# Optimization experiments

Measured on AMD Instinct MI355X. Metric: run time of the kernel, lower is better.

## Reference

```python
import jax, jax.numpy as jnp
import numpy as np

EPS = 1e-5

def _layernorm(x, w, b):
    # LayerNorm over (C,F,S) per batch element, affine params shape [C,F,S]
    m = jnp.mean(x, axis=(1, 2, 3), keepdims=True)
    v = jnp.mean((x - m) ** 2, axis=(1, 2, 3), keepdims=True)
    return (x - m) * jax.lax.rsqrt(v + EPS) * w + b

def _pconv(x, w, b):
    # 1x1 conv == channel GEMM: w [O,C], x [B,C,F,S]
    return jnp.einsum('oc,bcfs->bofs', w, x) + b[:, None, None]

def setup_inputs() -> dict:
    C, F, S, B = 64, 256, 256, 4
    key = jax.random.key(0)
    ks = jax.random.split(key, 16)
    sc = 0.05
    return {
        'x': jax.random.normal(ks[0], (B, C, F, S), jnp.float32),
        'ln1_w': jnp.ones((C, F, S), jnp.float32),
        'ln1_b': jnp.zeros((C, F, S), jnp.float32),
        'ln2_w': jnp.ones((C, F, S), jnp.float32),
        'ln2_b': jnp.zeros((C, F, S), jnp.float32),
        'w1': jax.random.normal(ks[1], (2 * C, C), jnp.float32) * sc,
        'b1': jnp.zeros((2 * C,), jnp.float32),
        'dw_w': jax.random.normal(ks[2], (2 * C,), jnp.float32) * sc + 1.0,
        'dw_b': jnp.zeros((2 * C,), jnp.float32),
        'attn_w1': jax.random.normal(ks[3], (C, C), jnp.float32) * sc,
        'attn_b1': jnp.zeros((C,), jnp.float32),
        'attn_w2': jax.random.normal(ks[4], (C, C), jnp.float32) * sc,
        'attn_b2': jnp.zeros((C,), jnp.float32),
        'w2': jax.random.normal(ks[5], (C, C), jnp.float32) * sc,
        'b2': jnp.zeros((C,), jnp.float32),
        'w3': jax.random.normal(ks[6], (2 * C, C), jnp.float32) * sc,
        'b3': jnp.zeros((2 * C,), jnp.float32),
        'w4': jax.random.normal(ks[7], (C, C), jnp.float32) * sc,
        'b4': jnp.zeros((C,), jnp.float32),
    }

def reference(x, ln1_w, ln1_b, ln2_w, ln2_b, w1, b1, dw_w, dw_b,
              attn_w1, attn_b1, attn_w2, attn_b2, w2, b2, w3, b3, w4, b4):
    # branch 1: norm -> 1x1 conv (C->2C) -> depthwise 1x1 -> GLU -> channel attn -> 1x1 conv
    h = _layernorm(x, ln1_w, ln1_b)
    h = _pconv(h, w1, b1)
    h = h * dw_w[:, None, None] + dw_b[:, None, None]  # 1x1 depthwise = per-channel affine
    a, g = jnp.split(h, 2, axis=1)
    h = a * jax.nn.sigmoid(g)  # GLU over channel dim
    # channel attention (SE-style, reduction_ratio=1)
    p = jnp.mean(h, axis=(2, 3))  # [B,C]
    s = jax.nn.sigmoid(jax.nn.relu(p @ attn_w1.T + attn_b1) @ attn_w2.T + attn_b2)
    h = h * s[:, :, None, None]
    h = _pconv(h, w2, b2)
    y = h + x
    # branch 2: norm -> 1x1 conv (C->2C) -> GLU -> 1x1 conv
    h2 = _layernorm(y, ln2_w, ln2_b)
    h2 = _pconv(h2, w3, b3)
    a2, g2 = jnp.split(h2, 2, axis=1)
    h2 = a2 * jax.nn.sigmoid(g2)
    h2 = _pconv(h2, w4, b4)
    return h2 + y
```

## Files before the change

kernel.cpp:

```cpp
#include <hip/hip_runtime.h>
#include <cstdint>
#include <cstddef>

#define CH 64
#define NP 65536
#define NPB 1024
constexpr float EPS_LN = 1e-5f;

using f32x4  = __attribute__((ext_vector_type(4))) float;
using bf16x8 = __attribute__((ext_vector_type(8))) short;
using s16x4  = __attribute__((ext_vector_type(4))) short;
using s16x2  = __attribute__((ext_vector_type(2))) short;

__device__ __forceinline__ short f2bf(float f){
  union { float f; uint32_t u; } v; v.f = f;
  uint32_t r = v.u + 0x7FFFu + ((v.u >> 16) & 1u);
  return (short)(r >> 16);
}
__device__ __forceinline__ float bf2f(short s){
  union { uint32_t u; float f; } v; v.u = ((uint32_t)(uint16_t)s) << 16;
  return v.f;
}
__device__ __forceinline__ float sigmoidf_(float x){ return 1.f/(1.f+__expf(-x)); }

__device__ __forceinline__ void lds_barrier(){
  asm volatile("s_waitcnt lgkmcnt(0)\n\ts_barrier" ::: "memory");
}

__global__ __launch_bounds__(256) void k_prep(
    const float* __restrict__ x,
    const float* __restrict__ w1, const float* __restrict__ w2,
    const float* __restrict__ w3, const float* __restrict__ w4,
    float* __restrict__ xstat, short* __restrict__ wbf)
{
  int blk = blockIdx.x, tid = threadIdx.x;
  if (blk < 1024) {
    int b = blk >> 8, chunk = blk & 255;
    const float* base = x + (size_t)b*CH*NP + (size_t)chunk*16384;
    float s = 0.f, s2 = 0.f;
    for (int i = tid*4; i < 16384; i += 1024) {
      f32x4 v = *(const f32x4*)(base + i);
      s  += v.x + v.y + v.z + v.w;
      s2 += v.x*v.x + v.y*v.y + v.z*v.z + v.w*v.w;
    }
    for (int d=1; d<64; d<<=1){ s += __shfl_xor(s,d,64); s2 += __shfl_xor(s2,d,64); }
    __shared__ float ls[8];
    int wv = tid>>6;
    if ((tid&63)==0){ ls[wv]=s; ls[4+wv]=s2; }
    __syncthreads();
    if (tid==0){
      xstat[blk*2]   = ls[0]+ls[1]+ls[2]+ls[3];
      xstat[blk*2+1] = ls[4]+ls[5]+ls[6]+ls[7];
    }
  } else {
    int wblk = blk - 1024;
    const float* src; short* dst; int off;
    if (wblk < 8)       { src = w1; dst = wbf;         off = wblk*1024; }
    else if (wblk < 12) { src = w2; dst = wbf + 8192;  off = (wblk-8)*1024; }
    else if (wblk < 20) { src = w3; dst = wbf + 12288; off = (wblk-12)*1024; }
    else                { src = w4; dst = wbf + 20480; off = (wblk-20)*1024; }
    for (int i = tid; i < 1024; i += 256) dst[off+i] = f2bf(src[off+i]);
  }
}

__global__ void k_fin1(const float* __restrict__ xstat, float* __restrict__ stats1){
  int b = threadIdx.x >> 6, lane = threadIdx.x & 63;
  float s=0.f, s2=0.f;
  #pragma unroll
  for (int j=0;j<4;j++){
    int i = b*256 + j*64 + lane;
    s += xstat[i*2]; s2 += xstat[i*2+1];
  }
  for (int d=1; d<64; d<<=1){ s += __shfl_xor(s,d,64); s2 += __shfl_xor(s2,d,64); }
  if (lane==0){
    float m = s*(1.f/4194304.f);
    float v = s2*(1.f/4194304.f) - m*m;
    stats1[b]=m; stats1[4+b]=rsqrtf(v+EPS_LN);
  }
}

__global__ __launch_bounds__(256,4) void k_branch1(
    const float* __restrict__ x, const float* __restrict__ lnw, const float* __restrict__ lnb,
    const short* __restrict__ w1bf, const float* __restrict__ b1,
    const float* __restrict__ dww, const float* __restrict__ dwb,
    const float* __restrict__ stats1, short* __restrict__ hglu, float* __restrict__ ppart)
{
  int blk = blockIdx.x;
  int b = blk >> 8;
  int tile0 = (blk & 255) * 4;
  int tid = threadIdx.x, wv = tid>>6, lane = tid&63, l = lane&15, q = lane>>4;
  int c_ = tid>>4, p4 = tid&15;
  float mean = stats1[b], rstd = stats1[4+b];
  const float* xb = x + (size_t)b*CH*NP;
  short* hb = hglu + (size_t)b*CH*NP;

  __shared__ __align__(16) short wlds[8192];
  __shared__ __align__(16) short lin[64*78];
  __shared__ float pacc[4][64];
  __shared__ __align__(16) float cc[128];

  #pragma unroll
  for (int g0=0; g0<4; g0++){
    int g = g0*256 + tid;
    int mt = g>>7, ks = (g>>6)&1, qq = (g>>4)&3, ll = g&15;
    int m = mt*16 + ll;
    float sc = dww[m];
    bf16x8 w8 = *(const bf16x8*)(w1bf + (m*CH + ks*32 + qq*8));
    #pragma unroll
    for (int j=0;j<8;j++) w8[j] = f2bf(bf2f(w8[j]) * sc);
    *(bf16x8*)(&wlds[g*8]) = w8;
  }
  if (tid < 128) cc[tid] = b1[tid]*dww[tid] + dwb[tid];

  f32x4 pX[4], pW[4], pB[4];
  #pragma unroll
  for (int it=0; it<4; it++){
    int c = it*16 + c_;
    size_t o = (size_t)c*NP + tile0*64 + p4*4;
    pX[it] = *(const f32x4*)(xb + o);
    pW[it] = *(const f32x4*)(lnw + o);
    pB[it] = *(const f32x4*)(lnb + o);
  }

  float rsum[16];
  #pragma unroll
  for (int i=0;i<16;i++) rsum[i] = 0.f;

  for (int t=0; t<4; t++){
    int pos0 = (tile0 + t)*64;
    #pragma unroll
    for (int it=0; it<4; it++){
      int c = it*16 + c_;
      s16x2 lo, hi;
      lo[0] = f2bf((pX[it][0]-mean)*rstd*pW[it][0] + pB[it][0]);
      lo[1] = f2bf((pX[it][1]-mean)*rstd*pW[it][1] + pB[it][1]);
      hi[0] = f2bf((pX[it][2]-mean)*rstd*pW[it][2] + pB[it][2]);
      hi[1] = f2bf((pX[it][3]-mean)*rstd*pW[it][3] + pB[it][3]);
      *(s16x2*)(&lin[c*78 + p4*4])     = lo;
      *(s16x2*)(&lin[c*78 + p4*4 + 2]) = hi;
    }
    if (t < 3){
      #pragma unroll
      for (int it=0; it<4; it++){
        int c = it*16 + c_;
        size_t o = (size_t)c*NP + pos0 + 64 + p4*4;
        pX[it] = *(const f32x4*)(xb + o);
        pW[it] = *(const f32x4*)(lnw + o);
        pB[it] = *(const f32x4*)(lnb + o);
      }
    }
    lds_barrier();

    bf16x8 bfrag[2];
    #pragma unroll
    for (int ks=0; ks<2; ks++)
      #pragma unroll
      for (int j=0; j<8; j++)
        bfrag[ks][j] = lin[(ks*32+q*8+j)*78 + wv*16 + l];

    f32x4 acc[8];
    #pragma unroll
    for (int mt=0; mt<8; mt++){
      f32x4 a = {0.f,0.f,0.f,0.f};
      #pragma unroll
      for (int ks=0; ks<2; ks++){
        bf16x8 af = *(const bf16x8*)(&wlds[(mt*128 + ks*64 + q*16 + l)*8]);
        a = __builtin_amdgcn_mfma_f32_16x16x32_bf16(af, bfrag[ks], a, 0, 0, 0);
      }
      acc[mt] = a;
    }

    int pos = pos0 + wv*16 + l;
    #pragma unroll
    for (int mt=0; mt<4; mt++){
      f32x4 ccA = *(const f32x4*)(&cc[mt*16 + q*4]);
      f32x4 ccG = *(const f32x4*)(&cc[64 + mt*16 + q*4]);
      s16x4 pk;
      #pragma unroll
      for (int r=0; r<4; r++){
        float av = acc[mt][r]   + ccA[r];
        float gv = acc[mt+4][r] + ccG[r];
        float h = av * sigmoidf_(gv);
        rsum[mt*4+r] += h;
        pk[r] = f2bf(h);
      }
      *(s16x4*)(hb + (size_t)pos*CH + mt*16 + q*4) = pk;
    }
    lds_barrier();
  }

  #pragma unroll
  for (int i=0;i<16;i++){
    float v = rsum[i];
    v += __shfl_xor(v,1,64); v += __shfl_xor(v,2,64);
    v += __shfl_xor(v,4,64); v += __shfl_xor(v,8,64);
    if (l==0) pacc[wv][(i>>2)*16 + q*4 + (i&3)] = v;
  }
  lds_barrier();
  if (tid < 64){
    float s = pacc[0][tid]+pacc[1][tid]+pacc[2][tid]+pacc[3][tid];
    ppart[((size_t)b*256 + (blk & 255))*64 + tid] = s;
  }
}

__global__ __launch_bounds__(1024) void k_attn(
    const float* __restrict__ ppart,
    const float* __restrict__ aw1, const float* __restrict__ ab1,
    const float* __restrict__ aw2, const float* __restrict__ ab2,
    const short* __restrict__ w2bf, short* __restrict__ w2s)
{
  int b = blockIdx.x, t = threadIdx.x;
  int c = t & 63, seg = t >> 6;
  __shared__ float awl1[64*65], awl2[64*65];
  __shared__ float pl[16][64];
  __shared__ float parr[64], t1a[64], sarr[64];

  #pragma unroll
  for (int k=0;k<4;k++){
    int i = t + k*1024;
    int row = i >> 6, col = i & 63;
    awl1[row*65 + col] = aw1[i];
    awl2[row*65 + col] = aw2[i];
  }
  const float* pb = ppart + (size_t)b*256*64;
  float s = 0.f;
  #pragma unroll
  for (int k=0;k<16;k++) s += pb[(seg*16 + k)*64 + c];
  pl[seg][c] = s;
  __syncthreads();
  if (t < 64){
    float acc = 0.f;
    #pragma unroll
    for (int j=0;j<16;j++) acc += pl[j][t];
    parr[t] = acc * (1.f/65536.f);
  }
  __syncthreads();
  if (t < 64){
    float acc = ab1[t];
    #pragma unroll
    for (int k=0;k<64;k++) acc += awl1[t*65+k]*parr[k];
    t1a[t] = fmaxf(acc, 0.f);
  }
  __syncthreads();
  if (t < 64){
    float acc = ab2[t];
    #pragma unroll
    for (int k=0;k<64;k++) acc += awl2[t*65+k]*t1a[k];
    sarr[t] = sigmoidf_(acc);
  }
  __syncthreads();
  #pragma unroll
  for (int k=0;k<4;k++){
    int i = t + k*1024;
    w2s[b*4096 + i] = f2bf(bf2f(w2bf[i]) * sarr[i & 63]);
  }
}

__global__ __launch_bounds__(256,4) void k_mid(
    const short* __restrict__ hglu, const short* __restrict__ w2s,
    const float* __restrict__ b2, const float* __restrict__ x,
    float* __restrict__ y, float* __restrict__ ystat)
{
  int blk = blockIdx.x;
  int b = blk >> 8;
  int tile0 = (blk & 255) * 4;
  int tid = threadIdx.x, wv = tid>>6, lane = tid&63, l = lane&15, q = lane>>4;
  int c_ = tid>>4, p4 = tid&15;
  const short* hb = hglu + (size_t)b*CH*NP;
  const float* xb = x + (size_t)b*CH*NP;
  float* yb = y + (size_t)b*CH*NP;
  int posl = wv*16 + l;

  __shared__ __align__(16) short w2l[4096];
  __shared__ __align__(16) float lout[64*65];

  #pragma unroll
  for (int g0=0; g0<2; g0++){
    int g = g0*256 + tid;
    int mt = g>>7, ks = (g>>6)&1, qq = (g>>4)&3, ll = g&15;
    *(bf16x8*)(&w2l[g*8]) = *(const bf16x8*)(w2s + b*4096 + (mt*16+ll)*CH + ks*32 + qq*8);
  }
  float b2v[4];
  #pragma unroll
  for (int it=0; it<4; it++) b2v[it] = b2[it*16 + c_];

  bf16x8 pH0, pH1; f32x4 pXr[4];
  {
    const short* hr = hb + (size_t)(tile0*64 + posl)*CH;
    pH0 = *(const bf16x8*)(hr + q*8);
    pH1 = *(const bf16x8*)(hr + 32 + q*8);
    #pragma unroll
    for (int it=0; it<4; it++)
      pXr[it] = *(const f32x4*)(xb + (size_t)(it*16+c_)*NP + tile0*64 + p4*4);
  }
  lds_barrier();

  float s1 = 0.f, s2 = 0.f;

  for (int t=0; t<4; t++){
    int pos0 = (tile0 + t)*64;
    bf16x8 h0 = pH0, h1 = pH1;
    if (t < 3){
      const short* hr = hb + (size_t)(pos0 + 64 + posl)*CH;
      pH0 = *(const bf16x8*)(hr + q*8);
      pH1 = *(const bf16x8*)(hr + 32 + q*8);
    }
    f32x4 acc[4];
    #pragma unroll
    for (int mt=0; mt<4; mt++){
      f32x4 a = {0.f,0.f,0.f,0.f};
      a = __builtin_amdgcn_mfma_f32_16x16x32_bf16(
            *(const bf16x8*)(&w2l[(mt*128 + 0*64 + q*16 + l)*8]), h0, a, 0,0,0);
      a = __builtin_amdgcn_mfma_f32_16x16x32_bf16(
            *(const bf16x8*)(&w2l[(mt*128 + 1*64 + q*16 + l)*8]), h1, a, 0,0,0);
      acc[mt] = a;
    }
    #pragma unroll
    for (int mt=0; mt<4; mt++)
      #pragma unroll
      for (int r=0; r<4; r++)
        lout[posl*65 + mt*16 + q*4 + r] = acc[mt][r];
    lds_barrier();

    f32x4 yv[4];
    #pragma unroll
    for (int it=0; it<4; it++){
      int c = it*16 + c_;
      #pragma unroll
      for (int j=0; j<4; j++){
        float v = lout[(p4*4+j)*65 + c] + b2v[it] + pXr[it][j];
        yv[it][j] = v; s1 += v; s2 += v*v;
      }
    }
    if (t < 3){
      #pragma unroll
      for (int it=0; it<4; it++)
        pXr[it] = *(const f32x4*)(xb + (size_t)(it*16+c_)*NP + pos0 + 64 + p4*4);
    }
    #pragma unroll
    for (int it=0; it<4; it++)
      *(f32x4*)(yb + (size_t)(it*16+c_)*NP + pos0 + p4*4) = yv[it];
    lds_barrier();
  }

  for (int d=1; d<64; d<<=1){ s1 += __shfl_xor(s1,d,64); s2 += __shfl_xor(s2,d,64); }
  __shared__ float red[8];
  if (lane==0){ red[wv]=s1; red[4+wv]=s2; }
  __syncthreads();
  if (tid==0){
    ystat[(size_t)blk*2]   = red[0]+red[1]+red[2]+red[3];
    ystat[(size_t)blk*2+1] = red[4]+red[5]+red[6]+red[7];
  }
}

__global__ void k_fin2(const float* __restrict__ ystat, float* __restrict__ stats2){
  int t = threadIdx.x;
  int b = t >> 6, lane = t & 63;
  float s=0.f, s2=0.f;
  #pragma unroll
  for (int j=0;j<4;j++){
    int e = b*256 + j*64 + lane;
    s  += ystat[e*2];
    s2 += ystat[e*2+1];
  }
  for (int d=1; d<64; d<<=1){ s += __shfl_xor(s,d,64); s2 += __shfl_xor(s2,d,64); }
  if (lane==0){
    float m = s*(1.f/4194304.f);
    float v = s2*(1.f/4194304.f) - m*m;
    stats2[b]=m; stats2[4+b]=rsqrtf(v+EPS_LN);
  }
}

__global__ __launch_bounds__(256,3) void k_branch2(
    float* __restrict__ yio, const float* __restrict__ lnw, const float* __restrict__ lnb,
    const short* __restrict__ w3bf, const float* __restrict__ b3,
    const short* __restrict__ w4bf, const float* __restrict__ b4,
    const float* __restrict__ stats2)
{
  int blk = blockIdx.x;
  int b = blk >> 8;
  int tile0 = (blk & 255) * 4;
  int tid = threadIdx.x, wv = tid>>6, lane = tid&63, l = lane&15, q = lane>>4;
  int c_ = tid>>4, p4 = tid&15;
  float mean = stats2[b], rstd = stats2[4+b];
  float* yb = yio + (size_t)b*CH*NP;
  int posl = wv*16 + l;

  __shared__ __align__(16) short w3l[8192];
  __shared__ __align__(16) short w4l[4096];
  __shared__ __align__(16) short lin[64*78];
  __shared__ __align__(16) char lun[64*65*4];
  short* lglu = (short*)lun;
  float* lout = (float*)lun;
  __shared__ __align__(16) float b3l[128];

  #pragma unroll
  for (int g0=0; g0<4; g0++){
    int g = g0*256 + tid;
    int mt = g>>7, ks = (g>>6)&1, qq = (g>>4)&3, ll = g&15;
    *(bf16x8*)(&w3l[g*8]) = *(const bf16x8*)(w3bf + ((mt*16+ll)*CH + ks*32 + qq*8));
  }
  #pragma unroll
  for (int g0=0; g0<2; g0++){
    int g = g0*256 + tid;
    int mt = g>>7, ks = (g>>6)&1, qq = (g>>4)&3, ll = g&15;
    *(bf16x8*)(&w4l[g*8]) = *(const bf16x8*)(w4bf + ((mt*16+ll)*CH + ks*32 + qq*8));
  }
  if (tid < 128) b3l[tid] = b3[tid];
  float b4v[4];
  #pragma unroll
  for (int it=0; it<4; it++) b4v[it] = b4[it*16 + c_];

  f32x4 pY[4], pW[4], pB[4];
  #pragma unroll
  for (int it=0; it<4; it++){
    int c = it*16 + c_;
    size_t o = (size_t)c*NP + tile0*64 + p4*4;
    pY[it] = *(const f32x4*)(yb + o);
    pW[it] = *(const f32x4*)(lnw + o);
    pB[it] = *(const f32x4*)(lnb + o);
  }

  for (int t=0; t<4; t++){
    int pos0 = (tile0 + t)*64;
    #pragma unroll
    for (int it=0; it<4; it++){
      int c = it*16 + c_;
      s16x2 lo, hi;
      lo[0] = f2bf((pY[it][0]-mean)*rstd*pW[it][0] + pB[it][0]);
      lo[1] = f2bf((pY[it][1]-mean)*rstd*pW[it][1] + pB[it][1]);
      hi[0] = f2bf((pY[it][2]-mean)*rstd*pW[it][2] + pB[it][2]);
      hi[1] = f2bf((pY[it][3]-mean)*rstd*pW[it][3] + pB[it][3]);
      *(s16x2*)(&lin[c*78 + p4*4])     = lo;
      *(s16x2*)(&lin[c*78 + p4*4 + 2]) = hi;
    }
    if (t < 3){
      #pragma unroll
      for (int it=0; it<4; it++){
        int c = it*16 + c_;
        size_t o = (size_t)c*NP + pos0 + 64 + p4*4;
        pW[it] = *(const f32x4*)(lnw + o);
        pB[it] = *(const f32x4*)(lnb + o);
      }
    }
    lds_barrier();

    bf16x8 bfrag[2];
    #pragma unroll
    for (int ks=0; ks<2; ks++)
      #pragma unroll
      for (int j=0; j<8; j++)
        bfrag[ks][j] = lin[(ks*32+q*8+j)*78 + wv*16 + l];

    f32x4 acc[8];
    #pragma unroll
    for (int mt=0; mt<8; mt++){
      f32x4 a = {0.f,0.f,0.f,0.f};
      #pragma unroll
      for (int ks=0; ks<2; ks++){
        bf16x8 af = *(const bf16x8*)(&w3l[(mt*128 + ks*64 + q*16 + l)*8]);
        a = __builtin_amdgcn_mfma_f32_16x16x32_bf16(af, bfrag[ks], a, 0, 0, 0);
      }
      acc[mt] = a;
    }

    #pragma unroll
    for (int mt=0; mt<4; mt++){
      f32x4 bA = *(const f32x4*)(&b3l[mt*16 + q*4]);
      f32x4 bG = *(const f32x4*)(&b3l[64 + mt*16 + q*4]);
      s16x4 pk;
      #pragma unroll
      for (int r=0; r<4; r++){
        float av = acc[mt][r]   + bA[r];
        float gv = acc[mt+4][r] + bG[r];
        pk[r] = f2bf(av * sigmoidf_(gv));
      }
      *(s16x4*)(&lglu[posl*72 + mt*16 + q*4]) = pk;
    }
    lds_barrier();

    bf16x8 pfrag[2];
    pfrag[0] = *(const bf16x8*)(&lglu[posl*72 + q*8]);
    pfrag[1] = *(const bf16x8*)(&lglu[posl*72 + 32 + q*8]);
    lds_barrier();

    f32x4 acc2[4];
    #pragma unroll
    for (int mt=0; mt<4; mt++){
      f32x4 a = {0.f,0.f,0.f,0.f};
      #pragma unroll
      for (int ks=0; ks<2; ks++){
        bf16x8 af = *(const bf16x8*)(&w4l[(mt*128 + ks*64 + q*16 + l)*8]);
        a = __builtin_amdgcn_mfma_f32_16x16x32_bf16(af, ks ? pfrag[1] : pfrag[0], a, 0, 0, 0);
      }
      acc2[mt] = a;
    }
    #pragma unroll
    for (int mt=0; mt<4; mt++)
      #pragma unroll
      for (int r=0; r<4; r++)
        lout[posl*65 + mt*16 + q*4 + r] = acc2[mt][r];
    lds_barrier();

    f32x4 yv[4];
    #pragma unroll
    for (int it=0; it<4; it++){
      int c = it*16 + c_;
      #pragma unroll
      for (int j=0; j<4; j++)
        yv[it][j] = lout[(p4*4+j)*65 + c] + b4v[it] + pY[it][j];
    }
    if (t < 3){
      #pragma unroll
      for (int it=0; it<4; it++){
        int c = it*16 + c_;
        pY[it] = *(const f32x4*)(yb + (size_t)c*NP + pos0 + 64 + p4*4);
      }
    }
    #pragma unroll
    for (int it=0; it<4; it++)
      *(f32x4*)(yb + (size_t)(it*16+c_)*NP + pos0 + p4*4) = yv[it];
  }
}

extern "C" void kernel_launch(void* const* d_in, const int* in_sizes, int n_in,
                              void* d_out, int out_size, void* d_ws, size_t ws_size,
                              hipStream_t stream){
  const float* x    = (const float*)d_in[0];
  const float* ln1w = (const float*)d_in[1];
  const float* ln1b = (const float*)d_in[2];
  const float* ln2w = (const float*)d_in[3];
  const float* ln2b = (const float*)d_in[4];
  const float* w1   = (const float*)d_in[5];
  const float* b1   = (const float*)d_in[6];
  const float* dww  = (const float*)d_in[7];
  const float* dwb  = (const float*)d_in[8];
  const float* aw1  = (const float*)d_in[9];
  const float* ab1  = (const float*)d_in[10];
  const float* aw2  = (const float*)d_in[11];
  const float* ab2  = (const float*)d_in[12];
  const float* w2   = (const float*)d_in[13];
  const float* b2   = (const float*)d_in[14];
  const float* w3   = (const float*)d_in[15];
  const float* b3   = (const float*)d_in[16];
  const float* w4   = (const float*)d_in[17];
  const float* b4   = (const float*)d_in[18];
  float* out = (float*)d_out;
  float* ws  = (float*)d_ws;

  float* xstat  = ws;
  float* stats1 = ws + 2048;
  float* ystat  = ws + 2112;
  float* stats2 = ws + 10304;
  short* wbf    = (short*)(ws + 10368);
  short* w2s    = (short*)(ws + 22656);
  float* ppart  = ws + 30848;
  short* hglu   = (short*)(ws + 292992);

  hipLaunchKernelGGL(k_prep,    dim3(1048), dim3(256),  0, stream, x, w1, w2, w3, w4, xstat, wbf);
  hipLaunchKernelGGL(k_fin1,    dim3(1),    dim3(256),  0, stream, xstat, stats1);
  hipLaunchKernelGGL(k_branch1, dim3(1024), dim3(256),  0, stream, x, ln1w, ln1b, wbf, b1, dww, dwb, stats1, hglu, ppart);
  hipLaunchKernelGGL(k_attn,    dim3(4),    dim3(1024), 0, stream, ppart, aw1, ab1, aw2, ab2, wbf + 8192, w2s);
  hipLaunchKernelGGL(k_mid,     dim3(1024), dim3(256),  0, stream, hglu, w2s, b2, x, out, ystat);
  hipLaunchKernelGGL(k_fin2,    dim3(1),    dim3(256),  0, stream, ystat, stats2);
  hipLaunchKernelGGL(k_branch2, dim3(1024), dim3(256),  0, stream, out, ln2w, ln2b, wbf + 12288, b3, wbf + 20480, b4, stats2);
}
```

Baseline: 281.5 us.

## Make each wave own its position tile and drop block barriers in GEMM loops

Restructures branch1, mid and branch2 so each wavefront loads, normalizes and transposes its own 16-position slice through a private LDS region. Block-wide barriers inside the loop become per-wave lgkmcnt waits. Per-wave LDS buffers are smaller, and branch2 is split across twice as many blocks. The intent is to remove s_barrier stalls and lift occupancy and parallelism, at the cost of narrower 64-byte global access segments per channel row and LN weight loads no longer prefetched.

```diff
diff --git a/kernel.cpp b/kernel.cpp
--- a/kernel.cpp
+++ b/kernel.cpp
@@ -4,13 +4,11 @@
 
 #define CH 64
 #define NP 65536
-#define NPB 1024
 constexpr float EPS_LN = 1e-5f;
 
 using f32x4  = __attribute__((ext_vector_type(4))) float;
 using bf16x8 = __attribute__((ext_vector_type(8))) short;
 using s16x4  = __attribute__((ext_vector_type(4))) short;
-using s16x2  = __attribute__((ext_vector_type(2))) short;
 
 __device__ __forceinline__ short f2bf(float f){
   union { float f; uint32_t u; } v; v.f = f;
@@ -25,6 +23,9 @@
 
 __device__ __forceinline__ void lds_barrier(){
   asm volatile("s_waitcnt lgkmcnt(0)\n\ts_barrier" ::: "memory");
+}
+__device__ __forceinline__ void wave_fence(){
+  asm volatile("s_waitcnt lgkmcnt(0)" ::: "memory");
 }
 
 __global__ __launch_bounds__(256) void k_prep(
@@ -87,17 +88,17 @@
 {
   int blk = blockIdx.x;
   int b = blk >> 8;
-  int tile0 = (blk & 255) * 4;
   int tid = threadIdx.x, wv = tid>>6, lane = tid&63, l = lane&15, q = lane>>4;
-  int c_ = tid>>4, p4 = tid&15;
+  int base = (blk & 255)*256 + wv*64;
   float mean = stats1[b], rstd = stats1[4+b];
   const float* xb = x + (size_t)b*CH*NP;
   short* hb = hglu + (size_t)b*CH*NP;
 
   __shared__ __align__(16) short wlds[8192];
-  __shared__ __align__(16) short lin[64*78];
+  __shared__ __align__(16) float cc[128];
   __shared__ float pacc[4][64];
-  __shared__ __align__(16) float cc[128];
+  __shared__ __align__(16) short linS[4][1280];
+  short* lin = linS[wv];
 
   #pragma unroll
   for (int g0=0; g0<4; g0++){
@@ -112,51 +113,43 @@
   }
   if (tid < 128) cc[tid] = b1[tid]*dww[tid] + dwb[tid];
 
-  f32x4 pX[4], pW[4], pB[4];
-  #pragma unroll
-  for (int it=0; it<4; it++){
-    int c = it*16 + c_;
-    size_t o = (size_t)c*NP + tile0*64 + p4*4;
-    pX[it] = *(const f32x4*)(xb + o);
-    pW[it] = *(const f32x4*)(lnw + o);
-    pB[it] = *(const f32x4*)(lnb + o);
-  }
+  f32x4 pX[4];
+  #pragma unroll
+  for (int it=0; it<4; it++)
+    pX[it] = *(const f32x4*)(xb + (size_t)(it*16+l)*NP + base + q*4);
+  lds_barrier();
 
   float rsum[16];
   #pragma unroll
-  for (int i=0;i<16;i++) rsum[i] = 0.f;
-
+  for (int i=0;i<16;i++) rsum[i]=0.f;
+
+  #pragma unroll
   for (int t=0; t<4; t++){
-    int pos0 = (tile0 + t)*64;
+    int pos_w = base + t*16;
     #pragma unroll
     for (int it=0; it<4; it++){
-      int c = it*16 + c_;
-      s16x2 lo, hi;
-      lo[0] = f2bf((pX[it][0]-mean)*rstd*pW[it][0] + pB[it][0]);
-      lo[1] = f2bf((pX[it][1]-mean)*rstd*pW[it][1] + pB[it][1]);
-      hi[0] = f2bf((pX[it][2]-mean)*rstd*pW[it][2] + pB[it][2]);
-      hi[1] = f2bf((pX[it][3]-mean)*rstd*pW[it][3] + pB[it][3]);
-      *(s16x2*)(&lin[c*78 + p4*4])     = lo;
-      *(s16x2*)(&lin[c*78 + p4*4 + 2]) = hi;
+      int c = it*16 + l;
+      size_t o = (size_t)c*NP + pos_w + q*4;
+      f32x4 lw4 = *(const f32x4*)(lnw + o);
+      f32x4 lb4 = *(const f32x4*)(lnb + o);
+      s16x4 pk;
+      #pragma unroll
+      for (int j=0;j<4;j++) pk[j] = f2bf((pX[it][j]-mean)*rstd*lw4[j] + lb4[j]);
+      *(s16x4*)(&lin[c*20 + q*4]) = pk;
     }
     if (t < 3){
       #pragma unroll
-      for (int it=0; it<4; it++){
-        int c = it*16 + c_;
-        size_t o = (size_t)c*NP + pos0 + 64 + p4*4;
-        pX[it] = *(const f32x4*)(xb + o);
-        pW[it] = *(const f32x4*)(lnw + o);
-        pB[it] = *(const f32x4*)(lnb + o);
-      }
-    }
-    lds_barrier();
+      for (int it=0; it<4; it++)
+        pX[it] = *(const f32x4*)(xb + (size_t)(it*16+l)*NP + pos_w + 16 + q*4);
+    }
+    wave_fence();
 
     bf16x8 bfrag[2];
     #pragma unroll
     for (int ks=0; ks<2; ks++)
       #pragma unroll
       for (int j=0; j<8; j++)
-        bfrag[ks][j] = lin[(ks*32+q*8+j)*78 + wv*16 + l];
+        bfrag[ks][j] = lin[(ks*32 + q*8 + j)*20 + l];
 
     f32x4 acc[8];
     #pragma unroll
@@ -170,7 +163,6 @@
       acc[mt] = a;
     }
 
-    int pos = pos0 + wv*16 + l;
     #pragma unroll
     for (int mt=0; mt<4; mt++){
       f32x4 ccA = *(const f32x4*)(&cc[mt*16 + q*4]);
@@ -184,9 +176,8 @@
         rsum[mt*4+r] += h;
         pk[r] = f2bf(h);
       }
-      *(s16x4*)(hb + (size_t)pos*CH + mt*16 + q*4) = pk;
-    }
-    lds_barrier();
+      *(s16x4*)(hb + (size_t)(pos_w + l)*CH + mt*16 + q*4) = pk;
+    }
   }
 
   #pragma unroll
@@ -196,7 +187,7 @@
     v += __shfl_xor(v,4,64); v += __shfl_xor(v,8,64);
     if (l==0) pacc[wv][(i>>2)*16 + q*4 + (i&3)] = v;
   }
-  lds_barrier();
+  __syncthreads();
   if (tid < 64){
     float s = pacc[0][tid]+pacc[1][tid]+pacc[2][tid]+pacc[3][tid];
     ppart[((size_t)b*256 + (blk & 255))*64 + tid] = s;
@@ -263,16 +254,15 @@
 {
   int blk = blockIdx.x;
   int b = blk >> 8;
-  int tile0 = (blk & 255) * 4;
   int tid = threadIdx.x, wv = tid>>6, lane = tid&63, l = lane&15, q = lane>>4;
-  int c_ = tid>>4, p4 = tid&15;
+  int base = (blk & 255)*256 + wv*64;
   const short* hb = hglu + (size_t)b*CH*NP;
   const float* xb = x + (size_t)b*CH*NP;
   float* yb = y + (size_t)b*CH*NP;
-  int posl = wv*16 + l;
 
   __shared__ __align__(16) short w2l[4096];
-  __shared__ __align__(16) float lout[64*65];
+  __shared__ __align__(16) float foutS[4][1088];
+  float* fout = foutS[wv];
 
   #pragma unroll
   for (int g0=0; g0<2; g0++){
@@ -282,26 +272,26 @@
   }
   float b2v[4];
   #pragma unroll
-  for (int it=0; it<4; it++) b2v[it] = b2[it*16 + c_];
-
-  bf16x8 pH0, pH1; f32x4 pXr[4];
+  for (int it=0; it<4; it++) b2v[it] = b2[it*16 + l];
+
+  bf16x8 pH0, pH1; f32x4 pX[4];
   {
-    const short* hr = hb + (size_t)(tile0*64 + posl)*CH;
+    const short* hr = hb + (size_t)(base + l)*CH;
     pH0 = *(const bf16x8*)(hr + q*8);
     pH1 = *(const bf16x8*)(hr + 32 + q*8);
     #pragma unroll
     for (int it=0; it<4; it++)
-      pXr[it] = *(const f32x4*)(xb + (size_t)(it*16+c_)*NP + tile0*64 + p4*4);
+      pX[it] = *(const f32x4*)(xb + (size_t)(it*16+l)*NP + base + q*4);
   }
   lds_barrier();
 
-  float s1 = 0.f, s2 = 0.f;
-
+  float s1=0.f, s2=0.f;
+  #pragma unroll
   for (int t=0; t<4; t++){
-    int pos0 = (tile0 + t)*64;
+    int pos_w = base + t*16;
     bf16x8 h0 = pH0, h1 = pH1;
     if (t < 3){
-      const short* hr = hb + (size_t)(pos0 + 64 + posl)*CH;
+      const short* hr = hb + (size_t)(pos_w + 16 + l)*CH;
       pH0 = *(const bf16x8*)(hr + q*8);
       pH1 = *(const bf16x8*)(hr + 32 + q*8);
     }
@@ -317,30 +307,27 @@
     }
     #pragma unroll
     for (int mt=0; mt<4; mt++)
-      #pragma unroll
-      for (int r=0; r<4; r++)
-        lout[posl*65 + mt*16 + q*4 + r] = acc[mt][r];
-    lds_barrier();
+      *(f32x4*)(&fout[l*68 + mt*16 + q*4]) = acc[mt];
+    wave_fence();
 
     f32x4 yv[4];
     #pragma unroll
     for (int it=0; it<4; it++){
-      int c = it*16 + c_;
-      #pragma unroll
-      for (int j=0; j<4; j++){
-        float v = lout[(p4*4+j)*65 + c] + b2v[it] + pXr[it][j];
+      int c = it*16 + l;
+      #pragma unroll
+      for (int j=0;j<4;j++){
+        float v = fout[(q*4+j)*68 + c] + b2v[it] + pX[it][j];
         yv[it][j] = v; s1 += v; s2 += v*v;
       }
     }
     if (t < 3){
       #pragma unroll
       for (int it=0; it<4; it++)
-        pXr[it] = *(const f32x4*)(xb + (size_t)(it*16+c_)*NP + pos0 + 64 + p4*4);
+        pX[it] = *(const f32x4*)(xb + (size_t)(it*16+l)*NP + pos_w + 16 + q*4);
     }
     #pragma unroll
     for (int it=0; it<4; it++)
-      *(f32x4*)(yb + (size_t)(it*16+c_)*NP + pos0 + p4*4) = yv[it];
-    lds_barrier();
+      *(f32x4*)(yb + (size_t)(it*16+l)*NP + pos_w + q*4) = yv[it];
   }
 
   for (int d=1; d<64; d<<=1){ s1 += __shfl_xor(s1,d,64); s2 += __shfl_xor(s2,d,64); }
@@ -378,21 +365,19 @@
     const float* __restrict__ stats2)
 {
   int blk = blockIdx.x;
-  int b = blk >> 8;
-  int tile0 = (blk & 255) * 4;
+  int b = blk >> 9;
   int tid = threadIdx.x, wv = tid>>6, lane = tid&63, l = lane&15, q = lane>>4;
-  int c_ = tid>>4, p4 = tid&15;
+  int base = (blk & 511)*128 + wv*32;
   float mean = stats2[b], rstd = stats2[4+b];
   float* yb = yio + (size_t)b*CH*NP;
-  int posl = wv*16 + l;
 
   __shared__ __align__(16) short w3l[8192];
   __shared__ __align__(16) short w4l[4096];
-  __shared__ __align__(16) short lin[64*78];
-  __shared__ __align__(16) char lun[64*65*4];
-  short* lglu = (short*)lun;
-  float* lout = (float*)lun;
   __shared__ __align__(16) float b3l[128];
+  __shared__ __align__(16) char uniS[4][4352];
+  short* lin  = (short*)uniS[wv];
+  short* glu  = (short*)uniS[wv];
+  float* fout = (float*)uniS[wv];
 
   #pragma unroll
   for (int g0=0; g0<4; g0++){
@@ -409,48 +394,42 @@
   if (tid < 128) b3l[tid] = b3[tid];
   float b4v[4];
   #pragma unroll
-  for (int it=0; it<4; it++) b4v[it] = b4[it*16 + c_];
-
-  f32x4 pY[4], pW[4], pB[4];
-  #pragma unroll
-  for (int it=0; it<4; it++){
-    int c = it*16 + c_;
-    size_t o = (size_t)c*NP + tile0*64 + p4*4;
-    pY[it] = *(const f32x4*)(yb + o);
-    pW[it] = *(const f32x4*)(lnw + o);
-    pB[it] = *(const f32x4*)(lnb + o);
-  }
-
-  for (int t=0; t<4; t++){
-    int pos0 = (tile0 + t)*64;
+  for (int it=0; it<4; it++) b4v[it] = b4[it*16 + l];
+
+  f32x4 pY[4];
+  #pragma unroll
+  for (int it=0; it<4; it++)
+    pY[it] = *(const f32x4*)(yb + (size_t)(it*16+l)*NP + base + q*4);
+  lds_barrier();
+
+  #pragma unroll
+  for (int t=0; t<2; t++){
+    int pos_w = base + t*16;
     #pragma unroll
     for (int it=0; it<4; it++){
-      int c = it*16 + c_;
-      s16x2 lo, hi;
-      lo[0] = f2bf((pY[it][0]-mean)*rstd*pW[it][0] + pB[it][0]);
-      lo[1] = f2bf((pY[it][1]-mean)*rstd*pW[it][1] + pB[it][1]);
-      hi[0] = f2bf((pY[it][2]-mean)*rstd*pW[it][2] + pB[it][2]);
-      hi[1] = f2bf((pY[it][3]-mean)*rstd*pW[it][3] + pB[it][3]);
-      *(s16x2*)(&lin[c*78 + p4*4])     = lo;
-      *(s16x2*)(&lin[c*78 + p4*4 + 2]) = hi;
-    }
-    if (t < 3){
-      #pragma unroll
-      for (int it=0; it<4; it++){
-        int c = it*16 + c_;
-        size_t o = (size_t)c*NP + pos0 + 64 + p4*4;
-        pW[it] = *(const f32x4*)(lnw + o);
-        pB[it] = *(const f32x4*)(lnb + o);
-      }
-    }
-    lds_barrier();
+      int c = it*16 + l;
+      size_t o = (size_t)c*NP + pos_w + q*4;
+      f32x4 lw4 = *(const f32x4*)(lnw + o);
+      f32x4 lb4 = *(const f32x4*)(lnb + o);
+      s16x4 pk;
+      #pragma unroll
+      for (int j=0;j<4;j++) pk[j] = f2bf((pY[it][j]-mean)*rstd*lw4[j] + lb4[j]);
+      *(s16x4*)(&lin[c*20 + q*4]) = pk;
+    }
+    f32x4 nY[4];
+    if (t < 1){
+      #pragma unroll
+      for (int it=0; it<4; it++)
+        nY[it] = *(const f32x4*)(yb + (size_t)(it*16+l)*NP + pos_w + 16 + q*4);
+    }
+    wave_fence();
 
     bf16x8 bfrag[2];
     #pragma unroll
     for (int ks=0; ks<2; ks++)
       #pragma unroll
       for (int j=0; j<8; j++)
-        bfrag[ks][j] = lin[(ks*32+q*8+j)*78 + wv*16 + l];
+        bfrag[ks][j] = lin[(ks*32 + q*8 + j)*20 + l];
 
     f32x4 acc[8];
     #pragma unroll
@@ -475,14 +454,13 @@
         float gv = acc[mt+4][r] + bG[r];
         pk[r] = f2bf(av * sigmoidf_(gv));
       }
-      *(s16x4*)(&lglu[posl*72 + mt*16 + q*4]) = pk;
-    }
-    lds_barrier();
+      *(s16x4*)(&glu[l*80 + mt*16 + q*4]) = pk;
+    }
+    wave_fence();
 
     bf16x8 pfrag[2];
-    pfrag[0] = *(const bf16x8*)(&lglu[posl*72 + q*8]);
-    pfrag[1] = *(const bf16x8*)(&lglu[posl*72 + 32 + q*8]);
-    lds_barrier();
+    pfrag[0] = *(const bf16x8*)(&glu[l*80 + q*8]);
+    pfrag[1] = *(const bf16x8*)(&glu[l*80 + 32 + q*8]);
 
     f32x4 acc2[4];
     #pragma unroll
@@ -497,29 +475,24 @@
     }
     #pragma unroll
     for (int mt=0; mt<4; mt++)
-      #pragma unroll
-      for (int r=0; r<4; r++)
-        lout[posl*65 + mt*16 + q*4 + r] = acc2[mt][r];
-    lds_barrier();
+      *(f32x4*)(&fout[l*68 + mt*16 + q*4]) = acc2[mt];
+    wave_fence();
 
     f32x4 yv[4];
     #pragma unroll
     for (int it=0; it<4; it++){
-      int c = it*16 + c_;
-      #pragma unroll
-      for (int j=0; j<4; j++)
-        yv[it][j] = lout[(p4*4+j)*65 + c] + b4v[it] + pY[it][j];
-    }
-    if (t < 3){
-      #pragma unroll
-      for (int it=0; it<4; it++){
-        int c = it*16 + c_;
-        pY[it] = *(const f32x4*)(yb + (size_t)c*NP + pos0 + 64 + p4*4);
-      }
+      int c = it*16 + l;
+      #pragma unroll
+      for (int j=0;j<4;j++)
+        yv[it][j] = fout[(q*4+j)*68 + c] + b4v[it] + pY[it][j];
     }
     #pragma unroll
     for (int it=0; it<4; it++)
-      *(f32x4*)(yb + (size_t)(it*16+c_)*NP + pos0 + p4*4) = yv[it];
+      *(f32x4*)(yb + (size_t)(it*16+l)*NP + pos_w + q*4) = yv[it];
+    if (t < 1){
+      #pragma unroll
+      for (int it=0; it<4; it++) pY[it] = nY[it];
+    }
   }
 }
 
@@ -563,5 +536,5 @@
   hipLaunchKernelGGL(k_attn,    dim3(4),    dim3(1024), 0, stream, ppart, aw1, ab1, aw2, ab2, wbf + 8192, w2s);
   hipLaunchKernelGGL(k_mid,     dim3(1024), dim3(256),  0, stream, hglu, w2s, b2, x, out, ystat);
   hipLaunchKernelGGL(k_fin2,    dim3(1),    dim3(256),  0, stream, ystat, stats2);
-  hipLaunchKernelGGL(k_branch2, dim3(1024), dim3(256),  0, stream, out, ln2w, ln2b, wbf + 12288, b3, wbf + 20480, b4, stats2);
-}
+  hipLaunchKernelGGL(k_branch2, dim3(2048), dim3(256),  0, stream, out, ln2w, ln2b, wbf + 12288, b3, wbf + 20480, b4, stats2);
+}
```

Result: slower. 341.0 us (+21.1%).
